# Optimization experiments

Hardware: AMD Instinct MI355X
Metric: run time of the kernel (lower is better)

Reference implementation:

```python
import jax, jax.numpy as jnp
import numpy as np

N = 50000
E = 800000
IN_CH = 256
HID = 32
HEADS = 4
OUT_CH = 40
NEG_SLOPE = 0.2
BN_EPS = 1e-5


def _gat_conv(x, W, att_src, att_dst, bias, src, dst, num_nodes, concat):
    # x: [N, F_in]; W: [F_in, H*C]; att_src/att_dst: [H, C]
    H, C = att_src.shape
    h = (x @ W).reshape(num_nodes, H, C)            # [N, H, C]
    a_src = (h * att_src[None]).sum(-1)             # [N, H]
    a_dst = (h * att_dst[None]).sum(-1)             # [N, H]
    e = jax.nn.leaky_relu(a_src[src] + a_dst[dst], NEG_SLOPE)  # [Etot, H]
    # segment softmax over incoming edges of each destination node
    m = jax.ops.segment_max(e, dst, num_segments=num_nodes)    # [N, H]
    ex = jnp.exp(e - m[dst])
    s = jax.ops.segment_sum(ex, dst, num_segments=num_nodes)   # [N, H]
    alpha = ex / (s[dst] + 1e-16)                   # [Etot, H]
    out = jax.ops.segment_sum(h[src] * alpha[:, :, None], dst,
                              num_segments=num_nodes)          # [N, H, C]
    out = out.reshape(num_nodes, H * C) if concat else out.mean(axis=1)
    return out + bias


def setup_inputs() -> dict:
    key = jax.random.key(0)
    ks = jax.random.split(key, 12)
    x = jax.random.normal(ks[0], (N, IN_CH), dtype=jnp.float32)
    edge_index = jax.random.randint(ks[1], (2, E), 0, N, dtype=jnp.int64)
    # layer 1: in -> heads*hid, concat
    W1 = jax.random.normal(ks[2], (IN_CH, HEADS * HID), dtype=jnp.float32) * (1.0 / np.sqrt(IN_CH))
    att_src1 = jax.random.normal(ks[3], (HEADS, HID), dtype=jnp.float32) * 0.1
    att_dst1 = jax.random.normal(ks[4], (HEADS, HID), dtype=jnp.float32) * 0.1
    b1 = jnp.zeros((HEADS * HID,), dtype=jnp.float32)
    # batch norm over hidden*heads features
    gamma = jnp.ones((HEADS * HID,), dtype=jnp.float32)
    beta = jnp.zeros((HEADS * HID,), dtype=jnp.float32)
    # layer 2: heads*hid -> out, heads=1, mean (concat=False)
    W2 = jax.random.normal(ks[5], (HEADS * HID, OUT_CH), dtype=jnp.float32) * (1.0 / np.sqrt(HEADS * HID))
    att_src2 = jax.random.normal(ks[6], (1, OUT_CH), dtype=jnp.float32) * 0.1
    att_dst2 = jax.random.normal(ks[7], (1, OUT_CH), dtype=jnp.float32) * 0.1
    b2 = jnp.zeros((OUT_CH,), dtype=jnp.float32)
    return {"x": x, "edge_index": edge_index, "W1": W1, "att_src1": att_src1,
            "att_dst1": att_dst1, "b1": b1, "gamma": gamma, "beta": beta,
            "W2": W2, "att_src2": att_src2, "att_dst2": att_dst2, "b2": b2}


def reference(x, edge_index, W1, att_src1, att_dst1, b1, gamma, beta,
              W2, att_src2, att_dst2, b2):
    num_nodes = x.shape[0]
    loops = jnp.arange(num_nodes, dtype=edge_index.dtype)
    src = jnp.concatenate([edge_index[0], loops])   # add self-loops (PyG default)
    dst = jnp.concatenate([edge_index[1], loops])
    h = _gat_conv(x, W1, att_src1, att_dst1, b1, src, dst, num_nodes, concat=True)
    # BatchNorm over nodes (training-mode batch statistics)
    mu = h.mean(axis=0)
    var = h.var(axis=0)
    h = (h - mu) * jax.lax.rsqrt(var + BN_EPS) * gamma + beta
    h = jax.nn.elu(h)
    out = _gat_conv(h, W2, att_src2, att_dst2, b2, src, dst, num_nodes, concat=False)
    return out
```

## Files before the change

kernel.cpp:

```cpp
#include <hip/hip_runtime.h>

#define NN 50000
#define EE 800000
#define ETOT 850000
#define FIN 256
#define F1 128
#define F2 40
#define CAP 48

typedef unsigned int u32;
typedef unsigned short u16;

static __device__ __forceinline__ u32 f2bf(float f) {
  u32 u = __float_as_uint(f);
  return (u + 0x7FFFu + ((u >> 16) & 1u)) >> 16;
}
#define BF_LO(u) __uint_as_float((u) << 16)
#define BF_HI(u) __uint_as_float((u) & 0xFFFF0000u)

__global__ __launch_bounds__(256) void fill_kernel(const int* __restrict__ ei,
                                                   int* __restrict__ cnt,
                                                   int* __restrict__ csr) {
  int i = blockIdx.x * 256 + threadIdx.x;
  if (i < EE / 4) {
    int e = i * 4;
    int4 s4 = *(const int4*)(ei + e);
    int4 d4 = *(const int4*)(ei + EE + e);
    int p0 = atomicAdd(cnt + d4.x, 1); if (p0 < CAP) csr[d4.x * CAP + p0] = s4.x;
    int p1 = atomicAdd(cnt + d4.y, 1); if (p1 < CAP) csr[d4.y * CAP + p1] = s4.y;
    int p2 = atomicAdd(cnt + d4.z, 1); if (p2 < CAP) csr[d4.z * CAP + p2] = s4.z;
    int p3 = atomicAdd(cnt + d4.w, 1); if (p3 < CAP) csr[d4.w * CAP + p3] = s4.w;
  } else {
    int n = i - EE / 4;
    if (n < NN) {
      int p = atomicAdd(cnt + n, 1);
      if (p < CAP) csr[n * CAP + p] = n;
    }
  }
}

__global__ __launch_bounds__(256) void gemm1_kernel(const float* __restrict__ x,
                                                    const float* __restrict__ W1,
                                                    const float* __restrict__ att_src,
                                                    const float* __restrict__ att_dst,
                                                    u32* __restrict__ h1bf,
                                                    float* __restrict__ a_src,
                                                    float* __restrict__ a_dst) {
  __shared__ float Alds[16 * 132];
  __shared__ float Blds[16 * 128];
  __shared__ float att_s[128], att_d[128];
  const int t = threadIdx.x;
  if (t < 128) { att_s[t] = att_src[t]; att_d[t] = att_dst[t]; }
  const int m0 = blockIdx.x * 128;
  const int arow = t >> 1;
  const int akk = (t & 1) * 8;
  const int brow = t >> 4;
  const int bc = (t & 15) * 8;
  const int ty = t >> 4;
  const int tx = t & 15;

  float acc[8][8];
#pragma unroll
  for (int i = 0; i < 8; ++i)
#pragma unroll
    for (int j = 0; j < 8; ++j) acc[i][j] = 0.f;

  for (int k0 = 0; k0 < FIN; k0 += 16) {
    float4 a0 = {0.f, 0.f, 0.f, 0.f}, a1 = {0.f, 0.f, 0.f, 0.f};
    int gr = m0 + arow;
    if (gr < NN) {
      a0 = *(const float4*)(x + (size_t)gr * FIN + k0 + akk);
      a1 = *(const float4*)(x + (size_t)gr * FIN + k0 + akk + 4);
    }
    float4 b0 = *(const float4*)(W1 + (size_t)(k0 + brow) * F1 + bc);
    float4 b1 = *(const float4*)(W1 + (size_t)(k0 + brow) * F1 + bc + 4);
    __syncthreads();
    Alds[(akk + 0) * 132 + arow] = a0.x;
    Alds[(akk + 1) * 132 + arow] = a0.y;
    Alds[(akk + 2) * 132 + arow] = a0.z;
    Alds[(akk + 3) * 132 + arow] = a0.w;
    Alds[(akk + 4) * 132 + arow] = a1.x;
    Alds[(akk + 5) * 132 + arow] = a1.y;
    Alds[(akk + 6) * 132 + arow] = a1.z;
    Alds[(akk + 7) * 132 + arow] = a1.w;
    *(float4*)(Blds + brow * 128 + bc) = b0;
    *(float4*)(Blds + brow * 128 + bc + 4) = b1;
    __syncthreads();
#pragma unroll
    for (int k = 0; k < 16; ++k) {
      float4 av0 = *(const float4*)(Alds + k * 132 + ty * 8);
      float4 av1 = *(const float4*)(Alds + k * 132 + ty * 8 + 4);
      float4 bv0 = *(const float4*)(Blds + k * 128 + tx * 8);
      float4 bv1 = *(const float4*)(Blds + k * 128 + tx * 8 + 4);
      float aa[8] = {av0.x, av0.y, av0.z, av0.w, av1.x, av1.y, av1.z, av1.w};
      float bb[8] = {bv0.x, bv0.y, bv0.z, bv0.w, bv1.x, bv1.y, bv1.z, bv1.w};
#pragma unroll
      for (int i = 0; i < 8; ++i)
#pragma unroll
        for (int j = 0; j < 8; ++j) acc[i][j] = fmaf(aa[i], bb[j], acc[i][j]);
    }
  }
#pragma unroll
  for (int i = 0; i < 8; ++i) {
    int gr = m0 + ty * 8 + i;
    if (gr < NN) {
      uint4 w;
      w.x = f2bf(acc[i][0]) | (f2bf(acc[i][1]) << 16);
      w.y = f2bf(acc[i][2]) | (f2bf(acc[i][3]) << 16);
      w.z = f2bf(acc[i][4]) | (f2bf(acc[i][5]) << 16);
      w.w = f2bf(acc[i][6]) | (f2bf(acc[i][7]) << 16);
      *(uint4*)(h1bf + (size_t)gr * 64 + tx * 4) = w;
    }
  }
#pragma unroll
  for (int i = 0; i < 8; ++i) {
    float ps = 0.f, pd = 0.f;
#pragma unroll
    for (int j = 0; j < 8; ++j) {
      int c = tx * 8 + j;
      ps += acc[i][j] * att_s[c];
      pd += acc[i][j] * att_d[c];
    }
    ps += __shfl_xor(ps, 1); pd += __shfl_xor(pd, 1);
    ps += __shfl_xor(ps, 2); pd += __shfl_xor(pd, 2);
    if ((tx & 3) == 0) {
      int gr = m0 + ty * 8 + i;
      if (gr < NN) {
        int head = tx >> 2;
        a_src[gr * 4 + head] = ps;
        a_dst[gr * 4 + head] = pd;
      }
    }
  }
}

__global__ __launch_bounds__(256) void gather1_kernel(const int* __restrict__ cnt,
                                                      const int* __restrict__ csr,
                                                      const float* __restrict__ a_src,
                                                      const float* __restrict__ a_dst,
                                                      const u32* __restrict__ h1bf,
                                                      const float* __restrict__ b1,
                                                      float* __restrict__ h1b,
                                                      float* __restrict__ bnsum,
                                                      float* __restrict__ bnsq) {
  __shared__ float bns[128], bnq[128];
  int t = threadIdx.x;
  if (t < 128) { bns[t] = 0.f; bnq[t] = 0.f; }
  __syncthreads();
  int n = blockIdx.x * 16 + (t >> 4);
  int l = t & 15;
  int head = l >> 2;
  int f0 = l * 8;
  float adst = a_dst[n * 4 + head];
  float acc[8] = {0.f, 0.f, 0.f, 0.f, 0.f, 0.f, 0.f, 0.f};
  float ssum = 0.f;
  const int* row = csr + n * CAP;
  int m = cnt[n]; if (m > CAP) m = CAP;
  int i = 0;
  for (; i + 3 < m; i += 4) {
    int4 s4 = *(const int4*)(row + i);
    float e0 = a_src[s4.x * 4 + head] + adst;
    float e1 = a_src[s4.y * 4 + head] + adst;
    float e2 = a_src[s4.z * 4 + head] + adst;
    float e3 = a_src[s4.w * 4 + head] + adst;
    uint4 q0 = *(const uint4*)(h1bf + (size_t)s4.x * 64 + l * 4);
    uint4 q1 = *(const uint4*)(h1bf + (size_t)s4.y * 64 + l * 4);
    uint4 q2 = *(const uint4*)(h1bf + (size_t)s4.z * 64 + l * 4);
    uint4 q3 = *(const uint4*)(h1bf + (size_t)s4.w * 64 + l * 4);
    e0 = e0 > 0.f ? e0 : 0.2f * e0;  float x0 = __expf(e0);
    e1 = e1 > 0.f ? e1 : 0.2f * e1;  float x1 = __expf(e1);
    e2 = e2 > 0.f ? e2 : 0.2f * e2;  float x2 = __expf(e2);
    e3 = e3 > 0.f ? e3 : 0.2f * e3;  float x3 = __expf(e3);
    acc[0] = fmaf(x0, BF_LO(q0.x), acc[0]); acc[1] = fmaf(x0, BF_HI(q0.x), acc[1]);
    acc[2] = fmaf(x0, BF_LO(q0.y), acc[2]); acc[3] = fmaf(x0, BF_HI(q0.y), acc[3]);
    acc[4] = fmaf(x0, BF_LO(q0.z), acc[4]); acc[5] = fmaf(x0, BF_HI(q0.z), acc[5]);
    acc[6] = fmaf(x0, BF_LO(q0.w), acc[6]); acc[7] = fmaf(x0, BF_HI(q0.w), acc[7]);
    acc[0] = fmaf(x1, BF_LO(q1.x), acc[0]); acc[1] = fmaf(x1, BF_HI(q1.x), acc[1]);
    acc[2] = fmaf(x1, BF_LO(q1.y), acc[2]); acc[3] = fmaf(x1, BF_HI(q1.y), acc[3]);
    acc[4] = fmaf(x1, BF_LO(q1.z), acc[4]); acc[5] = fmaf(x1, BF_HI(q1.z), acc[5]);
    acc[6] = fmaf(x1, BF_LO(q1.w), acc[6]); acc[7] = fmaf(x1, BF_HI(q1.w), acc[7]);
    acc[0] = fmaf(x2, BF_LO(q2.x), acc[0]); acc[1] = fmaf(x2, BF_HI(q2.x), acc[1]);
    acc[2] = fmaf(x2, BF_LO(q2.y), acc[2]); acc[3] = fmaf(x2, BF_HI(q2.y), acc[3]);
    acc[4] = fmaf(x2, BF_LO(q2.z), acc[4]); acc[5] = fmaf(x2, BF_HI(q2.z), acc[5]);
    acc[6] = fmaf(x2, BF_LO(q2.w), acc[6]); acc[7] = fmaf(x2, BF_HI(q2.w), acc[7]);
    acc[0] = fmaf(x3, BF_LO(q3.x), acc[0]); acc[1] = fmaf(x3, BF_HI(q3.x), acc[1]);
    acc[2] = fmaf(x3, BF_LO(q3.y), acc[2]); acc[3] = fmaf(x3, BF_HI(q3.y), acc[3]);
    acc[4] = fmaf(x3, BF_LO(q3.z), acc[4]); acc[5] = fmaf(x3, BF_HI(q3.z), acc[5]);
    acc[6] = fmaf(x3, BF_LO(q3.w), acc[6]); acc[7] = fmaf(x3, BF_HI(q3.w), acc[7]);
    ssum += x0 + x1 + x2 + x3;
  }
  for (; i < m; ++i) {
    int s0 = row[i];
    float e0 = a_src[s0 * 4 + head] + adst;
    e0 = e0 > 0.f ? e0 : 0.2f * e0;
    float x0 = __expf(e0);
    uint4 q = *(const uint4*)(h1bf + (size_t)s0 * 64 + l * 4);
    acc[0] = fmaf(x0, BF_LO(q.x), acc[0]); acc[1] = fmaf(x0, BF_HI(q.x), acc[1]);
    acc[2] = fmaf(x0, BF_LO(q.y), acc[2]); acc[3] = fmaf(x0, BF_HI(q.y), acc[3]);
    acc[4] = fmaf(x0, BF_LO(q.z), acc[4]); acc[5] = fmaf(x0, BF_HI(q.z), acc[5]);
    acc[6] = fmaf(x0, BF_LO(q.w), acc[6]); acc[7] = fmaf(x0, BF_HI(q.w), acc[7]);
    ssum += x0;
  }
  float inv = 1.f / (ssum + 1e-16f);
  float4 b0 = *(const float4*)(b1 + f0);
  float4 b4 = *(const float4*)(b1 + f0 + 4);
  float o[8];
  o[0] = acc[0] * inv + b0.x; o[1] = acc[1] * inv + b0.y;
  o[2] = acc[2] * inv + b0.z; o[3] = acc[3] * inv + b0.w;
  o[4] = acc[4] * inv + b4.x; o[5] = acc[5] * inv + b4.y;
  o[6] = acc[6] * inv + b4.z; o[7] = acc[7] * inv + b4.w;
  float4 w0 = {o[0], o[1], o[2], o[3]};
  float4 w1 = {o[4], o[5], o[6], o[7]};
  *(float4*)(h1b + (size_t)n * F1 + f0) = w0;
  *(float4*)(h1b + (size_t)n * F1 + f0 + 4) = w1;
#pragma unroll
  for (int j = 0; j < 8; ++j) {
    atomicAdd(&bns[f0 + j], o[j]);
    atomicAdd(&bnq[f0 + j], o[j] * o[j]);
  }
  __syncthreads();
  if (t < 128) {
    atomicAdd(bnsum + t, bns[t]);
    atomicAdd(bnsq + t, bnq[t]);
  }
}

__global__ __launch_bounds__(256) void gemm2_kernel(const float* __restrict__ hpre,
                                                    const float* __restrict__ W2,
                                                    const float* __restrict__ bnsum,
                                                    const float* __restrict__ bnsq,
                                                    const float* __restrict__ gamma,
                                                    const float* __restrict__ beta,
                                                    const float* __restrict__ att_src2,
                                                    const float* __restrict__ att_dst2,
                                                    u16* __restrict__ h2bf,
                                                    float* __restrict__ a_src2,
                                                    float* __restrict__ a_dst2) {
  __shared__ float Wlds[128 * 40];
  __shared__ float Alds[16 * 128];
  __shared__ float sc[128], sh[128];
  int t = threadIdx.x;
  for (int i = t; i < 128 * 40; i += 256) Wlds[i] = W2[i];
  if (t < 128) {
    const float invN = 1.f / (float)NN;
    float mu = bnsum[t] * invN;
    float var = bnsq[t] * invN - mu * mu;
    float s = gamma[t] * rsqrtf(var + 1e-5f);
    sc[t] = s;
    sh[t] = beta[t] - mu * s;
  }
  int tr = t >> 3;
  int tc = t & 7;
  float as5[5], ad5[5];
#pragma unroll
  for (int j = 0; j < 5; ++j) { as5[j] = att_src2[tc * 5 + j]; ad5[j] = att_dst2[tc * 5 + j]; }
  int n0 = blockIdx.x * 128;
  int lrow = t >> 1;
  int lkk = (t & 1) * 8;
  float acc[4][5];
#pragma unroll
  for (int i = 0; i < 4; ++i)
#pragma unroll
    for (int j = 0; j < 5; ++j) acc[i][j] = 0.f;

  for (int k0 = 0; k0 < F1; k0 += 16) {
    float av[8];
    int gn = n0 + lrow;
    if (gn < NN) {
      float4 v0 = *(const float4*)(hpre + (size_t)gn * F1 + k0 + lkk);
      float4 v1 = *(const float4*)(hpre + (size_t)gn * F1 + k0 + lkk + 4);
      av[0] = v0.x; av[1] = v0.y; av[2] = v0.z; av[3] = v0.w;
      av[4] = v1.x; av[5] = v1.y; av[6] = v1.z; av[7] = v1.w;
    } else {
#pragma unroll
      for (int j = 0; j < 8; ++j) av[j] = 0.f;
    }
    __syncthreads();
#pragma unroll
    for (int j = 0; j < 8; ++j) {
      int kg = k0 + lkk + j;
      float a = av[j] * sc[kg] + sh[kg];
      a = a > 0.f ? a : (__expf(a) - 1.f);
      Alds[(lkk + j) * 128 + lrow] = a;
    }
    __syncthreads();
#pragma unroll
    for (int k = 0; k < 16; ++k) {
      float4 a4 = *(const float4*)(Alds + k * 128 + tr * 4);
      float aa[4] = {a4.x, a4.y, a4.z, a4.w};
      float w[5];
#pragma unroll
      for (int j = 0; j < 5; ++j) w[j] = Wlds[(k0 + k) * 40 + tc * 5 + j];
#pragma unroll
      for (int i = 0; i < 4; ++i)
#pragma unroll
        for (int j = 0; j < 5; ++j) acc[i][j] = fmaf(aa[i], w[j], acc[i][j]);
    }
  }
#pragma unroll
  for (int i = 0; i < 4; ++i) {
    int gn = n0 + tr * 4 + i;
    if (gn < NN) {
#pragma unroll
      for (int j = 0; j < 5; ++j)
        h2bf[(size_t)gn * 64 + tc * 5 + j] = (u16)f2bf(acc[i][j]);
      if (tc < 6) {
        uint2 z = {0u, 0u};
        *(uint2*)((u32*)h2bf + (size_t)gn * 32 + 20 + 2 * tc) = z;
      }
    }
  }
#pragma unroll
  for (int i = 0; i < 4; ++i) {
    float ps = 0.f, pd = 0.f;
#pragma unroll
    for (int j = 0; j < 5; ++j) { ps += acc[i][j] * as5[j]; pd += acc[i][j] * ad5[j]; }
#pragma unroll
    for (int off = 1; off < 8; off <<= 1) {
      ps += __shfl_xor(ps, off);
      pd += __shfl_xor(pd, off);
    }
    if (tc == 0) {
      int gn = n0 + tr * 4 + i;
      if (gn < NN) { a_src2[gn] = ps; a_dst2[gn] = pd; }
    }
  }
}

__global__ __launch_bounds__(256) void gather2_kernel(const int* __restrict__ cnt,
                                                      const int* __restrict__ csr,
                                                      const float* __restrict__ a_src,
                                                      const float* __restrict__ a_dst,
                                                      const u32* __restrict__ h2bf,
                                                      const float* __restrict__ b2,
                                                      float* __restrict__ out) {
  int t = threadIdx.x;
  int n = blockIdx.x * 32 + (t >> 3);
  if (n >= NN) return;
  int l = t & 7;
  float adst = a_dst[n];
  float acc[8] = {0.f, 0.f, 0.f, 0.f, 0.f, 0.f, 0.f, 0.f};
  float ssum = 0.f;
  const int* row = csr + n * CAP;
  int m = cnt[n]; if (m > CAP) m = CAP;
  int i = 0;
  for (; i + 3 < m; i += 4) {
    int4 s4 = *(const int4*)(row + i);
    float e0 = a_src[s4.x] + adst;
    float e1 = a_src[s4.y] + adst;
    float e2 = a_src[s4.z] + adst;
    float e3 = a_src[s4.w] + adst;
    uint4 q0 = *(const uint4*)(h2bf + (size_t)s4.x * 32 + l * 4);
    uint4 q1 = *(const uint4*)(h2bf + (size_t)s4.y * 32 + l * 4);
    uint4 q2 = *(const uint4*)(h2bf + (size_t)s4.z * 32 + l * 4);
    uint4 q3 = *(const uint4*)(h2bf + (size_t)s4.w * 32 + l * 4);
    e0 = e0 > 0.f ? e0 : 0.2f * e0;  float x0 = __expf(e0);
    e1 = e1 > 0.f ? e1 : 0.2f * e1;  float x1 = __expf(e1);
    e2 = e2 > 0.f ? e2 : 0.2f * e2;  float x2 = __expf(e2);
    e3 = e3 > 0.f ? e3 : 0.2f * e3;  float x3 = __expf(e3);
    acc[0] = fmaf(x0, BF_LO(q0.x), acc[0]); acc[1] = fmaf(x0, BF_HI(q0.x), acc[1]);
    acc[2] = fmaf(x0, BF_LO(q0.y), acc[2]); acc[3] = fmaf(x0, BF_HI(q0.y), acc[3]);
    acc[4] = fmaf(x0, BF_LO(q0.z), acc[4]); acc[5] = fmaf(x0, BF_HI(q0.z), acc[5]);
    acc[6] = fmaf(x0, BF_LO(q0.w), acc[6]); acc[7] = fmaf(x0, BF_HI(q0.w), acc[7]);
    acc[0] = fmaf(x1, BF_LO(q1.x), acc[0]); acc[1] = fmaf(x1, BF_HI(q1.x), acc[1]);
    acc[2] = fmaf(x1, BF_LO(q1.y), acc[2]); acc[3] = fmaf(x1, BF_HI(q1.y), acc[3]);
    acc[4] = fmaf(x1, BF_LO(q1.z), acc[4]); acc[5] = fmaf(x1, BF_HI(q1.z), acc[5]);
    acc[6] = fmaf(x1, BF_LO(q1.w), acc[6]); acc[7] = fmaf(x1, BF_HI(q1.w), acc[7]);
    acc[0] = fmaf(x2, BF_LO(q2.x), acc[0]); acc[1] = fmaf(x2, BF_HI(q2.x), acc[1]);
    acc[2] = fmaf(x2, BF_LO(q2.y), acc[2]); acc[3] = fmaf(x2, BF_HI(q2.y), acc[3]);
    acc[4] = fmaf(x2, BF_LO(q2.z), acc[4]); acc[5] = fmaf(x2, BF_HI(q2.z), acc[5]);
    acc[6] = fmaf(x2, BF_LO(q2.w), acc[6]); acc[7] = fmaf(x2, BF_HI(q2.w), acc[7]);
    acc[0] = fmaf(x3, BF_LO(q3.x), acc[0]); acc[1] = fmaf(x3, BF_HI(q3.x), acc[1]);
    acc[2] = fmaf(x3, BF_LO(q3.y), acc[2]); acc[3] = fmaf(x3, BF_HI(q3.y), acc[3]);
    acc[4] = fmaf(x3, BF_LO(q3.z), acc[4]); acc[5] = fmaf(x3, BF_HI(q3.z), acc[5]);
    acc[6] = fmaf(x3, BF_LO(q3.w), acc[6]); acc[7] = fmaf(x3, BF_HI(q3.w), acc[7]);
    ssum += x0 + x1 + x2 + x3;
  }
  for (; i < m; ++i) {
    int s0 = row[i];
    float e0 = a_src[s0] + adst;
    e0 = e0 > 0.f ? e0 : 0.2f * e0;
    float x0 = __expf(e0);
    uint4 q = *(const uint4*)(h2bf + (size_t)s0 * 32 + l * 4);
    acc[0] = fmaf(x0, BF_LO(q.x), acc[0]); acc[1] = fmaf(x0, BF_HI(q.x), acc[1]);
    acc[2] = fmaf(x0, BF_LO(q.y), acc[2]); acc[3] = fmaf(x0, BF_HI(q.y), acc[3]);
    acc[4] = fmaf(x0, BF_LO(q.z), acc[4]); acc[5] = fmaf(x0, BF_HI(q.z), acc[5]);
    acc[6] = fmaf(x0, BF_LO(q.w), acc[6]); acc[7] = fmaf(x0, BF_HI(q.w), acc[7]);
    ssum += x0;
  }
  float inv = 1.f / (ssum + 1e-16f);
  if (l < 5) {
    float* op = out + (size_t)n * F2 + l * 8;
#pragma unroll
    for (int j = 0; j < 8; ++j) op[j] = acc[j] * inv + b2[l * 8 + j];
  }
}

extern "C" void kernel_launch(void* const* d_in, const int* in_sizes, int n_in,
                              void* d_out, int out_size, void* d_ws, size_t ws_size,
                              hipStream_t stream) {
  const float* x        = (const float*)d_in[0];
  const int*   ei       = (const int*)d_in[1];
  const float* W1       = (const float*)d_in[2];
  const float* att_src1 = (const float*)d_in[3];
  const float* att_dst1 = (const float*)d_in[4];
  const float* b1       = (const float*)d_in[5];
  const float* gamma    = (const float*)d_in[6];
  const float* beta     = (const float*)d_in[7];
  const float* W2       = (const float*)d_in[8];
  const float* att_src2 = (const float*)d_in[9];
  const float* att_dst2 = (const float*)d_in[10];
  const float* b2       = (const float*)d_in[11];
  float* out = (float*)d_out;

  int* cnt      = (int*)d_ws;
  float* bnsum  = (float*)(cnt + 50048);
  float* bnsq   = bnsum + 128;
  int* csr      = (int*)(bnsq + 128);
  u32* h1bf     = (u32*)(csr + NN * CAP);
  float* h1b    = (float*)(h1bf + 3200000);
  u32* h2bf     = (u32*)(h1b + 6400000);
  float* a_src1 = (float*)(h2bf + 1600000);
  float* a_dst1 = a_src1 + 200000;
  float* a_src2 = a_dst1 + 200000;
  float* a_dst2 = a_src2 + 50000;

  hipMemsetAsync(cnt, 0, (50048 + 256) * sizeof(int), stream);

  fill_kernel<<<(EE / 4 + NN + 255) / 256, 256, 0, stream>>>(ei, cnt, csr);

  gemm1_kernel<<<(NN + 127) / 128, 256, 0, stream>>>(x, W1, att_src1, att_dst1,
                                                     h1bf, a_src1, a_dst1);
  gather1_kernel<<<NN / 16, 256, 0, stream>>>(cnt, csr, a_src1, a_dst1,
                                              h1bf, b1, h1b, bnsum, bnsq);
  gemm2_kernel<<<(NN + 127) / 128, 256, 0, stream>>>(h1b, W2, bnsum, bnsq,
                                                     gamma, beta,
                                                     att_src2, att_dst2,
                                                     (u16*)h2bf, a_src2, a_dst2);
  gather2_kernel<<<(NN + 31) / 32, 256, 0, stream>>>(cnt, csr, a_src2, a_dst2,
                                                     h2bf, b2, out);
}
```

Baseline: 354.3 us.

## Fuse CSR fill into GEMM1 launch and shrink layer-2 bf16 row stride

Merges the edge-bucketing fill kernel into the first GEMM launch by appending extra blocks that do the atomic CSR build, so both run concurrently in one launch instead of back-to-back. Separately, layer-2 bf16 features are stored at a 40-element stride instead of padded 64, which drops the zero-padding writes and cuts gather bytes; the three idle lanes per node skip their loads. The fused kernel carries GEMM shared memory for fill blocks, which may limit occupancy of those blocks, and the tighter stride can make rows straddle cache lines differently.

```diff
diff --git a/kernel.cpp b/kernel.cpp
--- a/kernel.cpp
+++ b/kernel.cpp
@@ -7,6 +7,8 @@
 #define F1 128
 #define F2 40
 #define CAP 48
+#define G1B ((NN + 127) / 128)
+#define FILLB ((EE / 4 + NN + 255) / 256)
 
 typedef unsigned int u32;
 typedef unsigned short u16;
@@ -18,38 +20,41 @@
 #define BF_LO(u) __uint_as_float((u) << 16)
 #define BF_HI(u) __uint_as_float((u) & 0xFFFF0000u)
 
-__global__ __launch_bounds__(256) void fill_kernel(const int* __restrict__ ei,
-                                                   int* __restrict__ cnt,
-                                                   int* __restrict__ csr) {
-  int i = blockIdx.x * 256 + threadIdx.x;
-  if (i < EE / 4) {
-    int e = i * 4;
-    int4 s4 = *(const int4*)(ei + e);
-    int4 d4 = *(const int4*)(ei + EE + e);
-    int p0 = atomicAdd(cnt + d4.x, 1); if (p0 < CAP) csr[d4.x * CAP + p0] = s4.x;
-    int p1 = atomicAdd(cnt + d4.y, 1); if (p1 < CAP) csr[d4.y * CAP + p1] = s4.y;
-    int p2 = atomicAdd(cnt + d4.z, 1); if (p2 < CAP) csr[d4.z * CAP + p2] = s4.z;
-    int p3 = atomicAdd(cnt + d4.w, 1); if (p3 < CAP) csr[d4.w * CAP + p3] = s4.w;
-  } else {
-    int n = i - EE / 4;
-    if (n < NN) {
-      int p = atomicAdd(cnt + n, 1);
-      if (p < CAP) csr[n * CAP + p] = n;
-    }
-  }
-}
-
-__global__ __launch_bounds__(256) void gemm1_kernel(const float* __restrict__ x,
-                                                    const float* __restrict__ W1,
-                                                    const float* __restrict__ att_src,
-                                                    const float* __restrict__ att_dst,
-                                                    u32* __restrict__ h1bf,
-                                                    float* __restrict__ a_src,
-                                                    float* __restrict__ a_dst) {
+__global__ __launch_bounds__(256) void g1f_kernel(const float* __restrict__ x,
+                                                  const float* __restrict__ W1,
+                                                  const float* __restrict__ att_src,
+                                                  const float* __restrict__ att_dst,
+                                                  u32* __restrict__ h1bf,
+                                                  float* __restrict__ a_src,
+                                                  float* __restrict__ a_dst,
+                                                  const int* __restrict__ ei,
+                                                  int* __restrict__ cnt,
+                                                  int* __restrict__ csr) {
   __shared__ float Alds[16 * 132];
   __shared__ float Blds[16 * 128];
   __shared__ float att_s[128], att_d[128];
   const int t = threadIdx.x;
+
+  if (blockIdx.x >= G1B) {
+    int i = (blockIdx.x - G1B) * 256 + t;
+    if (i < EE / 4) {
+      int e = i * 4;
+      int4 s4 = *(const int4*)(ei + e);
+      int4 d4 = *(const int4*)(ei + EE + e);
+      int p0 = atomicAdd(cnt + d4.x, 1); if (p0 < CAP) csr[d4.x * CAP + p0] = s4.x;
+      int p1 = atomicAdd(cnt + d4.y, 1); if (p1 < CAP) csr[d4.y * CAP + p1] = s4.y;
+      int p2 = atomicAdd(cnt + d4.z, 1); if (p2 < CAP) csr[d4.z * CAP + p2] = s4.z;
+      int p3 = atomicAdd(cnt + d4.w, 1); if (p3 < CAP) csr[d4.w * CAP + p3] = s4.w;
+    } else {
+      int n = i - EE / 4;
+      if (n < NN) {
+        int p = atomicAdd(cnt + n, 1);
+        if (p < CAP) csr[n * CAP + p] = n;
+      }
+    }
+    return;
+  }
+
   if (t < 128) { att_s[t] = att_src[t]; att_d[t] = att_dst[t]; }
   const int m0 = blockIdx.x * 128;
   const int arow = t >> 1;
@@ -303,11 +308,7 @@
     if (gn < NN) {
 #pragma unroll
       for (int j = 0; j < 5; ++j)
-        h2bf[(size_t)gn * 64 + tc * 5 + j] = (u16)f2bf(acc[i][j]);
-      if (tc < 6) {
-        uint2 z = {0u, 0u};
-        *(uint2*)((u32*)h2bf + (size_t)gn * 32 + 20 + 2 * tc) = z;
-      }
+        h2bf[(size_t)gn * 40 + tc * 5 + j] = (u16)f2bf(acc[i][j]);
     }
   }
 #pragma unroll
@@ -338,11 +339,13 @@
   int n = blockIdx.x * 32 + (t >> 3);
   if (n >= NN) return;
   int l = t & 7;
+  bool act = (l < 5);
   float adst = a_dst[n];
   float acc[8] = {0.f, 0.f, 0.f, 0.f, 0.f, 0.f, 0.f, 0.f};
   float ssum = 0.f;
   const int* row = csr + n * CAP;
   int m = cnt[n]; if (m > CAP) m = CAP;
+  const uint4 zz = {0u, 0u, 0u, 0u};
   int i = 0;
   for (; i + 3 < m; i += 4) {
     int4 s4 = *(const int4*)(row + i);
@@ -350,10 +353,10 @@
     float e1 = a_src[s4.y] + adst;
     float e2 = a_src[s4.z] + adst;
     float e3 = a_src[s4.w] + adst;
-    uint4 q0 = *(const uint4*)(h2bf + (size_t)s4.x * 32 + l * 4);
-    uint4 q1 = *(const uint4*)(h2bf + (size_t)s4.y * 32 + l * 4);
-    uint4 q2 = *(const uint4*)(h2bf + (size_t)s4.z * 32 + l * 4);
-    uint4 q3 = *(const uint4*)(h2bf + (size_t)s4.w * 32 + l * 4);
+    uint4 q0 = act ? *(const uint4*)(h2bf + (size_t)s4.x * 20 + l * 4) : zz;
+    uint4 q1 = act ? *(const uint4*)(h2bf + (size_t)s4.y * 20 + l * 4) : zz;
+    uint4 q2 = act ? *(const uint4*)(h2bf + (size_t)s4.z * 20 + l * 4) : zz;
+    uint4 q3 = act ? *(const uint4*)(h2bf + (size_t)s4.w * 20 + l * 4) : zz;
     e0 = e0 > 0.f ? e0 : 0.2f * e0;  float x0 = __expf(e0);
     e1 = e1 > 0.f ? e1 : 0.2f * e1;  float x1 = __expf(e1);
     e2 = e2 > 0.f ? e2 : 0.2f * e2;  float x2 = __expf(e2);
@@ -381,7 +384,7 @@
     float e0 = a_src[s0] + adst;
     e0 = e0 > 0.f ? e0 : 0.2f * e0;
     float x0 = __expf(e0);
-    uint4 q = *(const uint4*)(h2bf + (size_t)s0 * 32 + l * 4);
+    uint4 q = act ? *(const uint4*)(h2bf + (size_t)s0 * 20 + l * 4) : zz;
     acc[0] = fmaf(x0, BF_LO(q.x), acc[0]); acc[1] = fmaf(x0, BF_HI(q.x), acc[1]);
     acc[2] = fmaf(x0, BF_LO(q.y), acc[2]); acc[3] = fmaf(x0, BF_HI(q.y), acc[3]);
     acc[4] = fmaf(x0, BF_LO(q.z), acc[4]); acc[5] = fmaf(x0, BF_HI(q.z), acc[5]);
@@ -389,7 +392,7 @@
     ssum += x0;
   }
   float inv = 1.f / (ssum + 1e-16f);
-  if (l < 5) {
+  if (act) {
     float* op = out + (size_t)n * F2 + l * 8;
 #pragma unroll
     for (int j = 0; j < 8; ++j) op[j] = acc[j] * inv + b2[l * 8 + j];
@@ -420,17 +423,16 @@
   u32* h1bf     = (u32*)(csr + NN * CAP);
   float* h1b    = (float*)(h1bf + 3200000);
   u32* h2bf     = (u32*)(h1b + 6400000);
-  float* a_src1 = (float*)(h2bf + 1600000);
+  float* a_src1 = (float*)(h2bf + 1000000);
   float* a_dst1 = a_src1 + 200000;
   float* a_src2 = a_dst1 + 200000;
   float* a_dst2 = a_src2 + 50000;
 
   hipMemsetAsync(cnt, 0, (50048 + 256) * sizeof(int), stream);
 
-  fill_kernel<<<(EE / 4 + NN + 255) / 256, 256, 0, stream>>>(ei, cnt, csr);
-
-  gemm1_kernel<<<(NN + 127) / 128, 256, 0, stream>>>(x, W1, att_src1, att_dst1,
-                                                     h1bf, a_src1, a_dst1);
+  g1f_kernel<<<G1B + FILLB, 256, 0, stream>>>(x, W1, att_src1, att_dst1,
+                                              h1bf, a_src1, a_dst1,
+                                              ei, cnt, csr);
   gather1_kernel<<<NN / 16, 256, 0, stream>>>(cnt, csr, a_src1, a_dst1,
                                               h1bf, b1, h1b, bnsum, bnsq);
   gemm2_kernel<<<(NN + 127) / 128, 256, 0, stream>>>(h1b, W2, bnsum, bnsq,
```

Result: faster. 329.7 us (-6.9%).
